# Kernel optimization log

Hardware: AMD Instinct MI355X
Metric: run time of the kernel (lower is better)

## Reference

```python
import jax, jax.numpy as jnp
import numpy as np

COUNT_CLIP_MAX = 1000.0

def _mlp2(x, w1, b1, w2, b2):
    # sg2im-style build_mlp with final_nonlinearity=True: relu after every linear
    h = jax.nn.relu(x @ w1 + b1)
    return jax.nn.relu(h @ w2 + b2)

def setup_inputs() -> dict:
    key = jax.random.key(0)
    ks = jax.random.split(key, 12)
    O, T, D, H = 100000, 400000, 128, 128
    D_out = D
    obj_vecs = jax.random.normal(ks[0], (O, D), dtype=jnp.float32)
    predi_vecs = jax.random.normal(ks[1], (T, D), dtype=jnp.float32)
    edges = jax.random.randint(ks[2], (T, 2), 0, O, dtype=jnp.int32)
    s = 0.02
    # net1: [3D, H, 2H + D_out]
    w1a = jax.random.normal(ks[3], (3 * D, H), dtype=jnp.float32) * s
    b1a = jnp.zeros((H,), dtype=jnp.float32)
    w1b = jax.random.normal(ks[4], (H, 2 * H + D_out), dtype=jnp.float32) * s
    b1b = jnp.zeros((2 * H + D_out,), dtype=jnp.float32)
    # net2: [H, H, D_out]
    w2a = jax.random.normal(ks[5], (H, H), dtype=jnp.float32) * s
    b2a = jnp.zeros((H,), dtype=jnp.float32)
    w2b = jax.random.normal(ks[6], (H, D_out), dtype=jnp.float32) * s
    b2b = jnp.zeros((D_out,), dtype=jnp.float32)
    return dict(obj_vecs=obj_vecs, predi_vecs=predi_vecs, edges=edges,
                w1a=w1a, b1a=b1a, w1b=w1b, b1b=b1b,
                w2a=w2a, b2a=b2a, w2b=w2b, b2b=b2b)

def reference(obj_vecs, predi_vecs, edges, w1a, b1a, w1b, b1b, w2a, b2a, w2b, b2b):
    O = obj_vecs.shape[0]
    H = w1a.shape[1]
    D_out = w2b.shape[1]
    s_idx = edges[:, 0]
    o_idx = edges[:, 1]
    # gather subject/object vectors, concat with predicate vecs: (T, 3D)
    cur_t_vecs = jnp.concatenate([obj_vecs[s_idx], predi_vecs, obj_vecs[o_idx]], axis=1)
    new_t_vecs = _mlp2(cur_t_vecs, w1a, b1a, w1b, b1b)  # (T, 2H + D_out)
    new_s_vecs = new_t_vecs[:, :H]
    new_p_vecs = new_t_vecs[:, H:H + D_out]
    new_o_vecs = new_t_vecs[:, H + D_out:2 * H + D_out]
    # scatter-add back to objects
    pooled = jnp.zeros((O, H), dtype=obj_vecs.dtype)
    pooled = pooled.at[s_idx].add(new_s_vecs).at[o_idx].add(new_o_vecs)
    # avg pooling: divide by clipped incidence counts
    ones = jnp.ones(s_idx.shape[0], dtype=obj_vecs.dtype)
    counts = jnp.zeros((O,), dtype=obj_vecs.dtype).at[s_idx].add(ones).at[o_idx].add(ones)
    counts = jnp.clip(counts, 1.0, COUNT_CLIP_MAX)
    pooled = pooled / counts[:, None]
    new_obj_vecs = _mlp2(pooled, w2a, b2a, w2b, b2b)  # (O, D_out)
    return new_obj_vecs, new_p_vecs
```

## Files before the change

### kernel.cpp

```cpp
#include <hip/hip_runtime.h>

typedef __attribute__((ext_vector_type(8))) short bf16x8;
typedef __attribute__((ext_vector_type(4))) float f32x4;
typedef __attribute__((ext_vector_type(4))) unsigned short u16x4;

#define MFMA __builtin_amdgcn_mfma_f32_16x16x32_bf16

__device__ __forceinline__ unsigned short f2bf(float x) {
    union { float f; unsigned u; } v; v.f = x;
    unsigned r = v.u + 0x7FFFu + ((v.u >> 16) & 1u);
    return (unsigned short)(r >> 16);
}
__device__ __forceinline__ float bf2f(unsigned short h) {
    union { unsigned u; float f; } v; v.u = ((unsigned)h) << 16;
    return v.f;
}

__global__ void pack_weights(const float* __restrict__ w1a, const float* __restrict__ w1b,
                             const float* __restrict__ w2a, const float* __restrict__ w2b,
                             unsigned short* __restrict__ pk)
{
    const int b = blockIdx.x, l = threadIdx.x;
    const float* W; int N, tile; unsigned short *ph, *pl;
    if (b < 96)       { W = w1a; N = 128; tile = b;       ph = pk;                 pl = pk + 96*512; }
    else if (b < 192) { W = w1b; N = 384; tile = b - 96;  ph = pk + 2*96*512;      pl = pk + 3*96*512; }
    else if (b < 224) { W = w2a; N = 128; tile = b - 192; ph = pk + 4*96*512;      pl = pk + 4*96*512 + 32*512; }
    else              { W = w2b; N = 128; tile = b - 224; ph = pk + 4*96*512 + 2*32*512; pl = pk + 4*96*512 + 3*32*512; }
    const int tpr = N / 16;
    const int kc = tile / tpr, ct = tile % tpr;
    bf16x8 hv, lv;
#pragma unroll
    for (int j = 0; j < 8; ++j) {
        int k = kc * 32 + (l >> 4) * 8 + j;
        int n = ct * 16 + (l & 15);
        float v = W[(size_t)k * N + n];
        unsigned short h = f2bf(v);
        hv[j] = (short)h;
        lv[j] = (short)f2bf(v - bf2f(h));
    }
    *(bf16x8*)&ph[(size_t)(tile * 64 + l) * 8] = hv;
    *(bf16x8*)&pl[(size_t)(tile * 64 + l) * 8] = lv;
}

__global__ __launch_bounds__(512, 4) void triple_mlp_mfma(
    const float* __restrict__ obj, const float* __restrict__ predi,
    const int* __restrict__ edges,
    const float* __restrict__ b1a, const float* __restrict__ b1b,
    const unsigned short* __restrict__ pk1a_h, const unsigned short* __restrict__ pk1a_l,
    const unsigned short* __restrict__ pk1b_h, const unsigned short* __restrict__ pk1b_l,
    float* __restrict__ pooled, float* __restrict__ out_p,
    float* __restrict__ counts, int T)
{
    __shared__ __align__(16) unsigned short Xh[64 * 128];
    __shared__ __align__(16) unsigned short Xl[64 * 128];
    __shared__ int sIdx[64], oIdx[64];

    const int tid = threadIdx.x;
    const int w = tid >> 6, l = tid & 63;
    const int rh = w & 1, cg = w >> 1;
    const int t0 = blockIdx.x * 64;

    if (tid < 64) {
        int t = t0 + tid; int tc = (t < T) ? t : (T - 1);
        sIdx[tid] = edges[2 * tc];
        oIdx[tid] = edges[2 * tc + 1];
    }
    __syncthreads();

    if (tid < 64)        { if (t0 + tid      < T) atomicAdd(&counts[sIdx[tid]],      1.0f); }
    else if (tid < 128)  { if (t0 + tid - 64 < T) atomicAdd(&counts[oIdx[tid - 64]], 1.0f); }

    f32x4 acc1[2][2];
#pragma unroll
    for (int i = 0; i < 2; ++i) { acc1[i][0] = (f32x4)0.0f; acc1[i][1] = (f32x4)0.0f; }

#pragma unroll
    for (int s = 0; s < 3; ++s) {
#pragma unroll
        for (int it = 0; it < 4; ++it) {
            int q = it * 512 + tid;
            int row = q >> 5, c4 = (q & 31) * 4;
            int t = t0 + row; int tc = (t < T) ? t : (T - 1);
            const float* src = (s == 0) ? obj   + (size_t)sIdx[row] * 128 + c4
                             : (s == 1) ? predi + (size_t)tc        * 128 + c4
                                        : obj   + (size_t)oIdx[row] * 128 + c4;
            float4 v = *(const float4*)src;
            u16x4 hv, lv;
            unsigned short h;
            h = f2bf(v.x); hv[0] = h; lv[0] = f2bf(v.x - bf2f(h));
            h = f2bf(v.y); hv[1] = h; lv[1] = f2bf(v.y - bf2f(h));
            h = f2bf(v.z); hv[2] = h; lv[2] = f2bf(v.z - bf2f(h));
            h = f2bf(v.w); hv[3] = h; lv[3] = f2bf(v.w - bf2f(h));
            int pc = row * 128 + (c4 ^ ((row & 7) << 3));
            *(u16x4*)&Xh[pc] = hv;
            *(u16x4*)&Xl[pc] = lv;
        }
        __syncthreads();

#pragma unroll
        for (int kc2 = 0; kc2 < 4; ++kc2) {
            const int kcg = s * 4 + kc2;
            bf16x8 ah[2], al[2];
#pragma unroll
            for (int rt = 0; rt < 2; ++rt) {
                int row = (rh * 2 + rt) * 16 + (l & 15);
                int col0 = kc2 * 32 + (l >> 4) * 8;
                int pc = row * 128 + (col0 ^ ((row & 7) << 3));
                ah[rt] = *(const bf16x8*)&Xh[pc];
                al[rt] = *(const bf16x8*)&Xl[pc];
            }
#pragma unroll
            for (int c2 = 0; c2 < 2; ++c2) {
                const int tile = kcg * 8 + cg * 2 + c2;
                bf16x8 bh = *(const bf16x8*)&pk1a_h[(size_t)(tile * 64 + l) * 8];
                bf16x8 bl = *(const bf16x8*)&pk1a_l[(size_t)(tile * 64 + l) * 8];
#pragma unroll
                for (int rt = 0; rt < 2; ++rt) {
                    acc1[rt][c2] = MFMA(ah[rt], bh, acc1[rt][c2], 0, 0, 0);
                    acc1[rt][c2] = MFMA(ah[rt], bl, acc1[rt][c2], 0, 0, 0);
                    acc1[rt][c2] = MFMA(al[rt], bh, acc1[rt][c2], 0, 0, 0);
                }
            }
        }
        __syncthreads();
    }

#pragma unroll
    for (int c2 = 0; c2 < 2; ++c2) {
        int col = cg * 32 + c2 * 16 + (l & 15);
        float bb = b1a[col];
#pragma unroll
        for (int rt = 0; rt < 2; ++rt) {
#pragma unroll
            for (int r = 0; r < 4; ++r) {
                int row = (rh * 2 + rt) * 16 + (l >> 4) * 4 + r;
                float h = fmaxf(acc1[rt][c2][r] + bb, 0.0f);
                unsigned short hh = f2bf(h);
                unsigned short hl = f2bf(h - bf2f(hh));
                int pc = row * 128 + (col ^ ((row & 7) << 3));
                Xh[pc] = hh; Xl[pc] = hl;
            }
        }
    }
    __syncthreads();

    f32x4 acc2[2][6];
#pragma unroll
    for (int i = 0; i < 2; ++i)
#pragma unroll
        for (int j = 0; j < 6; ++j) acc2[i][j] = (f32x4)0.0f;

#pragma unroll
    for (int kc = 0; kc < 4; ++kc) {
        bf16x8 ah[2], al[2];
#pragma unroll
        for (int rt = 0; rt < 2; ++rt) {
            int row = (rh * 2 + rt) * 16 + (l & 15);
            int col0 = kc * 32 + (l >> 4) * 8;
            int pc = row * 128 + (col0 ^ ((row & 7) << 3));
            ah[rt] = *(const bf16x8*)&Xh[pc];
            al[rt] = *(const bf16x8*)&Xl[pc];
        }
#pragma unroll
        for (int ct = 0; ct < 6; ++ct) {
            const int tile = kc * 24 + cg * 6 + ct;
            bf16x8 bh = *(const bf16x8*)&pk1b_h[(size_t)(tile * 64 + l) * 8];
            bf16x8 bl = *(const bf16x8*)&pk1b_l[(size_t)(tile * 64 + l) * 8];
#pragma unroll
            for (int rt = 0; rt < 2; ++rt) {
                acc2[rt][ct] = MFMA(ah[rt], bh, acc2[rt][ct], 0, 0, 0);
                acc2[rt][ct] = MFMA(ah[rt], bl, acc2[rt][ct], 0, 0, 0);
                acc2[rt][ct] = MFMA(al[rt], bh, acc2[rt][ct], 0, 0, 0);
            }
        }
    }

#pragma unroll
    for (int ct = 0; ct < 6; ++ct) {
        int col = cg * 96 + ct * 16 + (l & 15);
        float bb = b1b[col];
#pragma unroll
        for (int rt = 0; rt < 2; ++rt) {
#pragma unroll
            for (int r = 0; r < 4; ++r) {
                int row = (rh * 2 + rt) * 16 + (l >> 4) * 4 + r;
                if (t0 + row >= T) continue;
                float v = fmaxf(acc2[rt][ct][r] + bb, 0.0f);
                if (col < 128)
                    atomicAdd(&pooled[(size_t)sIdx[row] * 128 + col], v);
                else if (col < 256)
                    out_p[(size_t)(t0 + row) * 128 + (col - 128)] = v;
                else
                    atomicAdd(&pooled[(size_t)oIdx[row] * 128 + (col - 256)], v);
            }
        }
    }
}

__global__ __launch_bounds__(512, 4) void obj_mlp_mfma(
    const float* __restrict__ b2a, const float* __restrict__ b2b,
    const unsigned short* __restrict__ pk2a_h, const unsigned short* __restrict__ pk2a_l,
    const unsigned short* __restrict__ pk2b_h, const unsigned short* __restrict__ pk2b_l,
    float* __restrict__ io, const float* __restrict__ counts, int O)
{
    __shared__ __align__(16) unsigned short Xh[64 * 128];
    __shared__ __align__(16) unsigned short Xl[64 * 128];

    const int tid = threadIdx.x;
    const int w = tid >> 6, l = tid & 63;
    const int rh = w & 1, cg = w >> 1;
    const int r0 = blockIdx.x * 64;

#pragma unroll
    for (int it = 0; it < 4; ++it) {
        int q = it * 512 + tid;
        int row = q >> 5, c4 = (q & 31) * 4;
        int rg = r0 + row; if (rg > O - 1) rg = O - 1;
        float c = counts[rg];
        c = fminf(fmaxf(c, 1.0f), 1000.0f);
        float inv = 1.0f / c;
        float4 v = *(const float4*)&io[(size_t)rg * 128 + c4];
        v.x *= inv; v.y *= inv; v.z *= inv; v.w *= inv;
        u16x4 hv, lv;
        unsigned short h;
        h = f2bf(v.x); hv[0] = h; lv[0] = f2bf(v.x - bf2f(h));
        h = f2bf(v.y); hv[1] = h; lv[1] = f2bf(v.y - bf2f(h));
        h = f2bf(v.z); hv[2] = h; lv[2] = f2bf(v.z - bf2f(h));
        h = f2bf(v.w); hv[3] = h; lv[3] = f2bf(v.w - bf2f(h));
        int pc = row * 128 + (c4 ^ ((row & 7) << 3));
        *(u16x4*)&Xh[pc] = hv;
        *(u16x4*)&Xl[pc] = lv;
    }
    __syncthreads();

    f32x4 acc[2][2];
#pragma unroll
    for (int i = 0; i < 2; ++i) { acc[i][0] = (f32x4)0.0f; acc[i][1] = (f32x4)0.0f; }

#pragma unroll
    for (int kc = 0; kc < 4; ++kc) {
        bf16x8 ah[2], al[2];
#pragma unroll
        for (int rt = 0; rt < 2; ++rt) {
            int row = (rh * 2 + rt) * 16 + (l & 15);
            int col0 = kc * 32 + (l >> 4) * 8;
            int pc = row * 128 + (col0 ^ ((row & 7) << 3));
            ah[rt] = *(const bf16x8*)&Xh[pc];
            al[rt] = *(const bf16x8*)&Xl[pc];
        }
#pragma unroll
        for (int c2 = 0; c2 < 2; ++c2) {
            const int tile = kc * 8 + cg * 2 + c2;
            bf16x8 bh = *(const bf16x8*)&pk2a_h[(size_t)(tile * 64 + l) * 8];
            bf16x8 bl = *(const bf16x8*)&pk2a_l[(size_t)(tile * 64 + l) * 8];
#pragma unroll
            for (int rt = 0; rt < 2; ++rt) {
                acc[rt][c2] = MFMA(ah[rt], bh, acc[rt][c2], 0, 0, 0);
                acc[rt][c2] = MFMA(ah[rt], bl, acc[rt][c2], 0, 0, 0);
                acc[rt][c2] = MFMA(al[rt], bh, acc[rt][c2], 0, 0, 0);
            }
        }
    }
    __syncthreads();

#pragma unroll
    for (int c2 = 0; c2 < 2; ++c2) {
        int col = cg * 32 + c2 * 16 + (l & 15);
        float bb = b2a[col];
#pragma unroll
        for (int rt = 0; rt < 2; ++rt) {
#pragma unroll
            for (int r = 0; r < 4; ++r) {
                int row = (rh * 2 + rt) * 16 + (l >> 4) * 4 + r;
                float h = fmaxf(acc[rt][c2][r] + bb, 0.0f);
                unsigned short hh = f2bf(h);
                unsigned short hl = f2bf(h - bf2f(hh));
                int pc = row * 128 + (col ^ ((row & 7) << 3));
                Xh[pc] = hh; Xl[pc] = hl;
            }
        }
    }
    __syncthreads();

    f32x4 acc2[2][2];
#pragma unroll
    for (int i = 0; i < 2; ++i) { acc2[i][0] = (f32x4)0.0f; acc2[i][1] = (f32x4)0.0f; }

#pragma unroll
    for (int kc = 0; kc < 4; ++kc) {
        bf16x8 ah[2], al[2];
#pragma unroll
        for (int rt = 0; rt < 2; ++rt) {
            int row = (rh * 2 + rt) * 16 + (l & 15);
            int col0 = kc * 32 + (l >> 4) * 8;
            int pc = row * 128 + (col0 ^ ((row & 7) << 3));
            ah[rt] = *(const bf16x8*)&Xh[pc];
            al[rt] = *(const bf16x8*)&Xl[pc];
        }
#pragma unroll
        for (int c2 = 0; c2 < 2; ++c2) {
            const int tile = kc * 8 + cg * 2 + c2;
            bf16x8 bh = *(const bf16x8*)&pk2b_h[(size_t)(tile * 64 + l) * 8];
            bf16x8 bl = *(const bf16x8*)&pk2b_l[(size_t)(tile * 64 + l) * 8];
#pragma unroll
            for (int rt = 0; rt < 2; ++rt) {
                acc2[rt][c2] = MFMA(ah[rt], bh, acc2[rt][c2], 0, 0, 0);
                acc2[rt][c2] = MFMA(ah[rt], bl, acc2[rt][c2], 0, 0, 0);
                acc2[rt][c2] = MFMA(al[rt], bh, acc2[rt][c2], 0, 0, 0);
            }
        }
    }

#pragma unroll
    for (int c2 = 0; c2 < 2; ++c2) {
        int col = cg * 32 + c2 * 16 + (l & 15);
        float bb = b2b[col];
#pragma unroll
        for (int rt = 0; rt < 2; ++rt) {
#pragma unroll
            for (int r = 0; r < 4; ++r) {
                int row = (rh * 2 + rt) * 16 + (l >> 4) * 4 + r;
                if (r0 + row >= O) continue;
                float v = fmaxf(acc2[rt][c2][r] + bb, 0.0f);
                io[(size_t)(r0 + row) * 128 + col] = v;
            }
        }
    }
}

extern "C" void kernel_launch(void* const* d_in, const int* in_sizes, int n_in,
                              void* d_out, int out_size, void* d_ws, size_t ws_size,
                              hipStream_t stream) {
    const float* obj   = (const float*)d_in[0];
    const float* predi = (const float*)d_in[1];
    const int*   edges = (const int*)d_in[2];
    const float* w1a   = (const float*)d_in[3];
    const float* b1a   = (const float*)d_in[4];
    const float* w1b   = (const float*)d_in[5];
    const float* b1b   = (const float*)d_in[6];
    const float* w2a   = (const float*)d_in[7];
    const float* b2a   = (const float*)d_in[8];
    const float* w2b   = (const float*)d_in[9];
    const float* b2b   = (const float*)d_in[10];
    (void)n_in; (void)ws_size; (void)out_size;

    const int O = in_sizes[0] / 128;
    const int T = in_sizes[1] / 128;

    float* out    = (float*)d_out;
    float* pooled = out;
    float* out_p  = out + (size_t)O * 128;
    float* counts = (float*)d_ws;

    unsigned short* pk = (unsigned short*)(counts + O);
    unsigned short* pk1a_h = pk;
    unsigned short* pk1a_l = pk1a_h + 96 * 512;
    unsigned short* pk1b_h = pk1a_l + 96 * 512;
    unsigned short* pk1b_l = pk1b_h + 96 * 512;
    unsigned short* pk2a_h = pk1b_l + 96 * 512;
    unsigned short* pk2a_l = pk2a_h + 32 * 512;
    unsigned short* pk2b_h = pk2a_l + 32 * 512;
    unsigned short* pk2b_l = pk2b_h + 32 * 512;

    hipMemsetAsync(pooled, 0, (size_t)O * 128 * sizeof(float), stream);
    hipMemsetAsync(counts, 0, (size_t)O * sizeof(float), stream);

    pack_weights<<<256, 64, 0, stream>>>(w1a, w1b, w2a, w2b, pk);

    triple_mlp_mfma<<<(T + 63) / 64, 512, 0, stream>>>(
        obj, predi, edges, b1a, b1b,
        pk1a_h, pk1a_l, pk1b_h, pk1b_l,
        pooled, out_p, counts, T);

    obj_mlp_mfma<<<(O + 63) / 64, 512, 0, stream>>>(
        b2a, b2b, pk2a_h, pk2a_l, pk2b_h, pk2b_l,
        pooled, counts, O);
}
```

Measured before the change: 984.0 us.

## Precompute per-object first-layer projections and gather them per edge

Splits the first linear layer by input block: the subject and object parts of W1a are applied once per object in a new kernel, writing a per-object table. The edge kernel then gathers and sums these projections, adding only the predicate GEMM. This cuts the per-edge first-layer matmul work to a third. In exchange it adds a large workspace table write and read, and requires enough workspace, with a fallback to the old path otherwise.

```diff
diff --git a/kernel.cpp b/kernel.cpp
--- a/kernel.cpp
+++ b/kernel.cpp
@@ -14,6 +14,460 @@
 __device__ __forceinline__ float bf2f(unsigned short h) {
     union { unsigned u; float f; } v; v.u = ((unsigned)h) << 16;
     return v.f;
+}
+
+__global__ void pack_new(const float* __restrict__ w1a, const float* __restrict__ w1b,
+                         const float* __restrict__ w2a, const float* __restrict__ w2b,
+                         unsigned short* __restrict__ pk)
+{
+    const int b = blockIdx.x, l = threadIdx.x;
+    unsigned short* ph;
+    unsigned short* pl;
+    int tile;
+    bf16x8 hv, lv;
+
+    if (b < 64) {
+        tile = b;
+        ph = pk; pl = pk + 64 * 512;
+        int kc = tile >> 4, ct = tile & 15;
+#pragma unroll
+        for (int j = 0; j < 8; ++j) {
+            int k = kc * 32 + (l >> 4) * 8 + j;
+            int n = ct * 16 + (l & 15);
+            float v = (n < 128) ? w1a[(size_t)k * 128 + n]
+                                : w1a[(size_t)(256 + k) * 128 + (n - 128)];
+            unsigned short h = f2bf(v);
+            hv[j] = (short)h; lv[j] = (short)f2bf(v - bf2f(h));
+        }
+    } else if (b < 96) {
+        tile = b - 64;
+        ph = pk + 2 * 64 * 512; pl = ph + 32 * 512;
+        int kc = tile >> 3, ct = tile & 7;
+#pragma unroll
+        for (int j = 0; j < 8; ++j) {
+            int k = kc * 32 + (l >> 4) * 8 + j;
+            int n = ct * 16 + (l & 15);
+            float v = w1a[(size_t)(128 + k) * 128 + n];
+            unsigned short h = f2bf(v);
+            hv[j] = (short)h; lv[j] = (short)f2bf(v - bf2f(h));
+        }
+    } else if (b < 192) {
+        tile = b - 96;
+        ph = pk + 2 * 64 * 512 + 2 * 32 * 512; pl = ph + 96 * 512;
+        int kc = tile / 24, ct = tile % 24;
+#pragma unroll
+        for (int j = 0; j < 8; ++j) {
+            int k = kc * 32 + (l >> 4) * 8 + j;
+            int n = ct * 16 + (l & 15);
+            float v = w1b[(size_t)k * 384 + n];
+            unsigned short h = f2bf(v);
+            hv[j] = (short)h; lv[j] = (short)f2bf(v - bf2f(h));
+        }
+    } else if (b < 224) {
+        tile = b - 192;
+        ph = pk + 2 * 64 * 512 + 2 * 32 * 512 + 2 * 96 * 512; pl = ph + 32 * 512;
+        int kc = tile >> 3, ct = tile & 7;
+#pragma unroll
+        for (int j = 0; j < 8; ++j) {
+            int k = kc * 32 + (l >> 4) * 8 + j;
+            int n = ct * 16 + (l & 15);
+            float v = w2a[(size_t)k * 128 + n];
+            unsigned short h = f2bf(v);
+            hv[j] = (short)h; lv[j] = (short)f2bf(v - bf2f(h));
+        }
+    } else {
+        tile = b - 224;
+        ph = pk + 2 * 64 * 512 + 2 * 32 * 512 + 2 * 96 * 512 + 2 * 32 * 512; pl = ph + 32 * 512;
+        int kc = tile >> 3, ct = tile & 7;
+#pragma unroll
+        for (int j = 0; j < 8; ++j) {
+            int k = kc * 32 + (l >> 4) * 8 + j;
+            int n = ct * 16 + (l & 15);
+            float v = w2b[(size_t)k * 128 + n];
+            unsigned short h = f2bf(v);
+            hv[j] = (short)h; lv[j] = (short)f2bf(v - bf2f(h));
+        }
+    }
+    *(bf16x8*)&ph[(size_t)(tile * 64 + l) * 8] = hv;
+    *(bf16x8*)&pl[(size_t)(tile * 64 + l) * 8] = lv;
+}
+
+__global__ __launch_bounds__(512, 4) void obj_pre_kernel(
+    const float* __restrict__ obj,
+    const unsigned short* __restrict__ pkc_h, const unsigned short* __restrict__ pkc_l,
+    float* __restrict__ A_tb, int O)
+{
+    __shared__ __align__(16) unsigned short Xh[64 * 128];
+    __shared__ __align__(16) unsigned short Xl[64 * 128];
+
+    const int tid = threadIdx.x;
+    const int w = tid >> 6, l = tid & 63;
+    const int rh = w & 1, cg = w >> 1;
+    const int r0 = blockIdx.x * 64;
+
+#pragma unroll
+    for (int it = 0; it < 4; ++it) {
+        int q = it * 512 + tid;
+        int row = q >> 5, c4 = (q & 31) * 4;
+        int rg = r0 + row; if (rg > O - 1) rg = O - 1;
+        float4 v = *(const float4*)&obj[(size_t)rg * 128 + c4];
+        u16x4 hv, lv; unsigned short h;
+        h = f2bf(v.x); hv[0] = h; lv[0] = f2bf(v.x - bf2f(h));
+        h = f2bf(v.y); hv[1] = h; lv[1] = f2bf(v.y - bf2f(h));
+        h = f2bf(v.z); hv[2] = h; lv[2] = f2bf(v.z - bf2f(h));
+        h = f2bf(v.w); hv[3] = h; lv[3] = f2bf(v.w - bf2f(h));
+        int pc = row * 128 + (c4 ^ ((row & 7) << 3));
+        *(u16x4*)&Xh[pc] = hv;
+        *(u16x4*)&Xl[pc] = lv;
+    }
+    __syncthreads();
+
+    f32x4 acc[2][4];
+#pragma unroll
+    for (int i = 0; i < 2; ++i)
+#pragma unroll
+        for (int j = 0; j < 4; ++j) acc[i][j] = (f32x4)0.0f;
+
+#pragma unroll
+    for (int kc = 0; kc < 4; ++kc) {
+        bf16x8 ah[2], al[2];
+#pragma unroll
+        for (int rt = 0; rt < 2; ++rt) {
+            int row = (rh * 2 + rt) * 16 + (l & 15);
+            int col0 = kc * 32 + (l >> 4) * 8;
+            int pc = row * 128 + (col0 ^ ((row & 7) << 3));
+            ah[rt] = *(const bf16x8*)&Xh[pc];
+            al[rt] = *(const bf16x8*)&Xl[pc];
+        }
+#pragma unroll
+        for (int ct = 0; ct < 4; ++ct) {
+            const int tile = kc * 16 + cg * 4 + ct;
+            bf16x8 bh = *(const bf16x8*)&pkc_h[(size_t)(tile * 64 + l) * 8];
+            bf16x8 bl = *(const bf16x8*)&pkc_l[(size_t)(tile * 64 + l) * 8];
+#pragma unroll
+            for (int rt = 0; rt < 2; ++rt) {
+                acc[rt][ct] = MFMA(ah[rt], bh, acc[rt][ct], 0, 0, 0);
+                acc[rt][ct] = MFMA(ah[rt], bl, acc[rt][ct], 0, 0, 0);
+                acc[rt][ct] = MFMA(al[rt], bh, acc[rt][ct], 0, 0, 0);
+            }
+        }
+    }
+
+#pragma unroll
+    for (int ct = 0; ct < 4; ++ct) {
+        int col = cg * 64 + ct * 16 + (l & 15);
+#pragma unroll
+        for (int rt = 0; rt < 2; ++rt) {
+#pragma unroll
+            for (int r = 0; r < 4; ++r) {
+                int row = (rh * 2 + rt) * 16 + (l >> 4) * 4 + r;
+                if (r0 + row < O)
+                    A_tb[(size_t)(r0 + row) * 256 + col] = acc[rt][ct][r];
+            }
+        }
+    }
+}
+
+__global__ __launch_bounds__(512, 4) void triple_mlp_mfma2(
+    const float* __restrict__ A_tb, const float* __restrict__ predi,
+    const int* __restrict__ edges,
+    const float* __restrict__ b1a, const float* __restrict__ b1b,
+    const unsigned short* __restrict__ pkm_h, const unsigned short* __restrict__ pkm_l,
+    const unsigned short* __restrict__ pk1b_h, const unsigned short* __restrict__ pk1b_l,
+    float* __restrict__ pooled, float* __restrict__ out_p,
+    float* __restrict__ counts, int T)
+{
+    __shared__ __align__(16) char SB[64 * 132 * 4];
+    float (*G)[132] = (float (*)[132])SB;
+    unsigned short* Xh = (unsigned short*)SB;
+    unsigned short* Xl = (unsigned short*)(SB + 64 * 128 * 2);
+    __shared__ int sIdx[64], oIdx[64];
+
+    const int tid = threadIdx.x;
+    const int w = tid >> 6, l = tid & 63;
+    const int rh = w & 1, cg = w >> 1;
+    const int t0 = blockIdx.x * 64;
+
+    if (tid < 64) {
+        int t = t0 + tid; int tc = (t < T) ? t : (T - 1);
+        sIdx[tid] = edges[2 * tc];
+        oIdx[tid] = edges[2 * tc + 1];
+    }
+    __syncthreads();
+
+    if (tid < 64)        { if (t0 + tid      < T) atomicAdd(&counts[sIdx[tid]],      1.0f); }
+    else if (tid < 128)  { if (t0 + tid - 64 < T) atomicAdd(&counts[oIdx[tid - 64]], 1.0f); }
+
+#pragma unroll
+    for (int it = 0; it < 4; ++it) {
+        int q = it * 512 + tid;
+        int row = q >> 5, c4 = (q & 31) * 4;
+        float4 a = *(const float4*)&A_tb[(size_t)sIdx[row] * 256 + c4];
+        float4 b = *(const float4*)&A_tb[(size_t)oIdx[row] * 256 + 128 + c4];
+        float4 bb = *(const float4*)&b1a[c4];
+        float4 g;
+        g.x = a.x + b.x + bb.x; g.y = a.y + b.y + bb.y;
+        g.z = a.z + b.z + bb.z; g.w = a.w + b.w + bb.w;
+        *(float4*)&G[row][c4] = g;
+    }
+    __syncthreads();
+
+    f32x4 acc1[2][2];
+#pragma unroll
+    for (int rt = 0; rt < 2; ++rt)
+#pragma unroll
+        for (int c2 = 0; c2 < 2; ++c2) {
+            int col = cg * 32 + c2 * 16 + (l & 15);
+#pragma unroll
+            for (int r = 0; r < 4; ++r) {
+                int row = (rh * 2 + rt) * 16 + (l >> 4) * 4 + r;
+                acc1[rt][c2][r] = G[row][col];
+            }
+        }
+    __syncthreads();
+
+#pragma unroll
+    for (int it = 0; it < 4; ++it) {
+        int q = it * 512 + tid;
+        int row = q >> 5, c4 = (q & 31) * 4;
+        int t = t0 + row; int tc = (t < T) ? t : (T - 1);
+        float4 v = *(const float4*)&predi[(size_t)tc * 128 + c4];
+        u16x4 hv, lv; unsigned short h;
+        h = f2bf(v.x); hv[0] = h; lv[0] = f2bf(v.x - bf2f(h));
+        h = f2bf(v.y); hv[1] = h; lv[1] = f2bf(v.y - bf2f(h));
+        h = f2bf(v.z); hv[2] = h; lv[2] = f2bf(v.z - bf2f(h));
+        h = f2bf(v.w); hv[3] = h; lv[3] = f2bf(v.w - bf2f(h));
+        int pc = row * 128 + (c4 ^ ((row & 7) << 3));
+        *(u16x4*)&Xh[pc] = hv;
+        *(u16x4*)&Xl[pc] = lv;
+    }
+    __syncthreads();
+
+#pragma unroll
+    for (int kc = 0; kc < 4; ++kc) {
+        bf16x8 ah[2], al[2];
+#pragma unroll
+        for (int rt = 0; rt < 2; ++rt) {
+            int row = (rh * 2 + rt) * 16 + (l & 15);
+            int col0 = kc * 32 + (l >> 4) * 8;
+            int pc = row * 128 + (col0 ^ ((row & 7) << 3));
+            ah[rt] = *(const bf16x8*)&Xh[pc];
+            al[rt] = *(const bf16x8*)&Xl[pc];
+        }
+#pragma unroll
+        for (int c2 = 0; c2 < 2; ++c2) {
+            const int tile = kc * 8 + cg * 2 + c2;
+            bf16x8 bh = *(const bf16x8*)&pkm_h[(size_t)(tile * 64 + l) * 8];
+            bf16x8 bl = *(const bf16x8*)&pkm_l[(size_t)(tile * 64 + l) * 8];
+#pragma unroll
+            for (int rt = 0; rt < 2; ++rt) {
+                acc1[rt][c2] = MFMA(ah[rt], bh, acc1[rt][c2], 0, 0, 0);
+                acc1[rt][c2] = MFMA(ah[rt], bl, acc1[rt][c2], 0, 0, 0);
+                acc1[rt][c2] = MFMA(al[rt], bh, acc1[rt][c2], 0, 0, 0);
+            }
+        }
+    }
+    __syncthreads();
+
+#pragma unroll
+    for (int c2 = 0; c2 < 2; ++c2) {
+        int col = cg * 32 + c2 * 16 + (l & 15);
+#pragma unroll
+        for (int rt = 0; rt < 2; ++rt) {
+#pragma unroll
+            for (int r = 0; r < 4; ++r) {
+                int row = (rh * 2 + rt) * 16 + (l >> 4) * 4 + r;
+                float h = fmaxf(acc1[rt][c2][r], 0.0f);
+                unsigned short hh = f2bf(h);
+                unsigned short hl = f2bf(h - bf2f(hh));
+                int pc = row * 128 + (col ^ ((row & 7) << 3));
+                Xh[pc] = hh; Xl[pc] = hl;
+            }
+        }
+    }
+    __syncthreads();
+
+    f32x4 acc2[2][6];
+#pragma unroll
+    for (int i = 0; i < 2; ++i)
+#pragma unroll
+        for (int j = 0; j < 6; ++j) acc2[i][j] = (f32x4)0.0f;
+
+#pragma unroll
+    for (int kc = 0; kc < 4; ++kc) {
+        bf16x8 ah[2], al[2];
+#pragma unroll
+        for (int rt = 0; rt < 2; ++rt) {
+            int row = (rh * 2 + rt) * 16 + (l & 15);
+            int col0 = kc * 32 + (l >> 4) * 8;
+            int pc = row * 128 + (col0 ^ ((row & 7) << 3));
+            ah[rt] = *(const bf16x8*)&Xh[pc];
+            al[rt] = *(const bf16x8*)&Xl[pc];
+        }
+#pragma unroll
+        for (int ct = 0; ct < 6; ++ct) {
+            const int tile = kc * 24 + cg * 6 + ct;
+            bf16x8 bh = *(const bf16x8*)&pk1b_h[(size_t)(tile * 64 + l) * 8];
+            bf16x8 bl = *(const bf16x8*)&pk1b_l[(size_t)(tile * 64 + l) * 8];
+#pragma unroll
+            for (int rt = 0; rt < 2; ++rt) {
+                acc2[rt][ct] = MFMA(ah[rt], bh, acc2[rt][ct], 0, 0, 0);
+                acc2[rt][ct] = MFMA(ah[rt], bl, acc2[rt][ct], 0, 0, 0);
+                acc2[rt][ct] = MFMA(al[rt], bh, acc2[rt][ct], 0, 0, 0);
+            }
+        }
+    }
+
+#pragma unroll
+    for (int ct = 0; ct < 6; ++ct) {
+        int col = cg * 96 + ct * 16 + (l & 15);
+        float bb = b1b[col];
+#pragma unroll
+        for (int rt = 0; rt < 2; ++rt) {
+#pragma unroll
+            for (int r = 0; r < 4; ++r) {
+                int row = (rh * 2 + rt) * 16 + (l >> 4) * 4 + r;
+                if (t0 + row >= T) continue;
+                float v = fmaxf(acc2[rt][ct][r] + bb, 0.0f);
+                if (col < 128)
+                    atomicAdd(&pooled[(size_t)sIdx[row] * 128 + col], v);
+                else if (col < 256)
+                    out_p[(size_t)(t0 + row) * 128 + (col - 128)] = v;
+                else
+                    atomicAdd(&pooled[(size_t)oIdx[row] * 128 + (col - 256)], v);
+            }
+        }
+    }
+}
+
+__global__ __launch_bounds__(512, 4) void obj_mlp_mfma(
+    const float* __restrict__ b2a, const float* __restrict__ b2b,
+    const unsigned short* __restrict__ pk2a_h, const unsigned short* __restrict__ pk2a_l,
+    const unsigned short* __restrict__ pk2b_h, const unsigned short* __restrict__ pk2b_l,
+    float* __restrict__ io, const float* __restrict__ counts, int O)
+{
+    __shared__ __align__(16) unsigned short Xh[64 * 128];
+    __shared__ __align__(16) unsigned short Xl[64 * 128];
+
+    const int tid = threadIdx.x;
+    const int w = tid >> 6, l = tid & 63;
+    const int rh = w & 1, cg = w >> 1;
+    const int r0 = blockIdx.x * 64;
+
+#pragma unroll
+    for (int it = 0; it < 4; ++it) {
+        int q = it * 512 + tid;
+        int row = q >> 5, c4 = (q & 31) * 4;
+        int rg = r0 + row; if (rg > O - 1) rg = O - 1;
+        float c = counts[rg];
+        c = fminf(fmaxf(c, 1.0f), 1000.0f);
+        float inv = 1.0f / c;
+        float4 v = *(const float4*)&io[(size_t)rg * 128 + c4];
+        v.x *= inv; v.y *= inv; v.z *= inv; v.w *= inv;
+        u16x4 hv, lv; unsigned short h;
+        h = f2bf(v.x); hv[0] = h; lv[0] = f2bf(v.x - bf2f(h));
+        h = f2bf(v.y); hv[1] = h; lv[1] = f2bf(v.y - bf2f(h));
+        h = f2bf(v.z); hv[2] = h; lv[2] = f2bf(v.z - bf2f(h));
+        h = f2bf(v.w); hv[3] = h; lv[3] = f2bf(v.w - bf2f(h));
+        int pc = row * 128 + (c4 ^ ((row & 7) << 3));
+        *(u16x4*)&Xh[pc] = hv;
+        *(u16x4*)&Xl[pc] = lv;
+    }
+    __syncthreads();
+
+    f32x4 acc[2][2];
+#pragma unroll
+    for (int i = 0; i < 2; ++i) { acc[i][0] = (f32x4)0.0f; acc[i][1] = (f32x4)0.0f; }
+
+#pragma unroll
+    for (int kc = 0; kc < 4; ++kc) {
+        bf16x8 ah[2], al[2];
+#pragma unroll
+        for (int rt = 0; rt < 2; ++rt) {
+            int row = (rh * 2 + rt) * 16 + (l & 15);
+            int col0 = kc * 32 + (l >> 4) * 8;
+            int pc = row * 128 + (col0 ^ ((row & 7) << 3));
+            ah[rt] = *(const bf16x8*)&Xh[pc];
+            al[rt] = *(const bf16x8*)&Xl[pc];
+        }
+#pragma unroll
+        for (int c2 = 0; c2 < 2; ++c2) {
+            const int tile = kc * 8 + cg * 2 + c2;
+            bf16x8 bh = *(const bf16x8*)&pk2a_h[(size_t)(tile * 64 + l) * 8];
+            bf16x8 bl = *(const bf16x8*)&pk2a_l[(size_t)(tile * 64 + l) * 8];
+#pragma unroll
+            for (int rt = 0; rt < 2; ++rt) {
+                acc[rt][c2] = MFMA(ah[rt], bh, acc[rt][c2], 0, 0, 0);
+                acc[rt][c2] = MFMA(ah[rt], bl, acc[rt][c2], 0, 0, 0);
+                acc[rt][c2] = MFMA(al[rt], bh, acc[rt][c2], 0, 0, 0);
+            }
+        }
+    }
+    __syncthreads();
+
+#pragma unroll
+    for (int c2 = 0; c2 < 2; ++c2) {
+        int col = cg * 32 + c2 * 16 + (l & 15);
+        float bb = b2a[col];
+#pragma unroll
+        for (int rt = 0; rt < 2; ++rt) {
+#pragma unroll
+            for (int r = 0; r < 4; ++r) {
+                int row = (rh * 2 + rt) * 16 + (l >> 4) * 4 + r;
+                float h = fmaxf(acc[rt][c2][r] + bb, 0.0f);
+                unsigned short hh = f2bf(h);
+                unsigned short hl = f2bf(h - bf2f(hh));
+                int pc = row * 128 + (col ^ ((row & 7) << 3));
+                Xh[pc] = hh; Xl[pc] = hl;
+            }
+        }
+    }
+    __syncthreads();
+
+    f32x4 acc2[2][2];
+#pragma unroll
+    for (int i = 0; i < 2; ++i) { acc2[i][0] = (f32x4)0.0f; acc2[i][1] = (f32x4)0.0f; }
+
+#pragma unroll
+    for (int kc = 0; kc < 4; ++kc) {
+        bf16x8 ah[2], al[2];
+#pragma unroll
+        for (int rt = 0; rt < 2; ++rt) {
+            int row = (rh * 2 + rt) * 16 + (l & 15);
+            int col0 = kc * 32 + (l >> 4) * 8;
+            int pc = row * 128 + (col0 ^ ((row & 7) << 3));
+            ah[rt] = *(const bf16x8*)&Xh[pc];
+            al[rt] = *(const bf16x8*)&Xl[pc];
+        }
+#pragma unroll
+        for (int c2 = 0; c2 < 2; ++c2) {
+            const int tile = kc * 8 + cg * 2 + c2;
+            bf16x8 bh = *(const bf16x8*)&pk2b_h[(size_t)(tile * 64 + l) * 8];
+            bf16x8 bl = *(const bf16x8*)&pk2b_l[(size_t)(tile * 64 + l) * 8];
+#pragma unroll
+            for (int rt = 0; rt < 2; ++rt) {
+                acc2[rt][c2] = MFMA(ah[rt], bh, acc2[rt][c2], 0, 0, 0);
+                acc2[rt][c2] = MFMA(ah[rt], bl, acc2[rt][c2], 0, 0, 0);
+                acc2[rt][c2] = MFMA(al[rt], bh, acc2[rt][c2], 0, 0, 0);
+            }
+        }
+    }
+
+#pragma unroll
+    for (int c2 = 0; c2 < 2; ++c2) {
+        int col = cg * 32 + c2 * 16 + (l & 15);
+        float bb = b2b[col];
+#pragma unroll
+        for (int rt = 0; rt < 2; ++rt) {
+#pragma unroll
+            for (int r = 0; r < 4; ++r) {
+                int row = (rh * 2 + rt) * 16 + (l >> 4) * 4 + r;
+                if (r0 + row >= O) continue;
+                float v = fmaxf(acc2[rt][c2][r] + bb, 0.0f);
+                io[(size_t)(r0 + row) * 128 + col] = v;
+            }
+        }
+    }
 }
 
 __global__ void pack_weights(const float* __restrict__ w1a, const float* __restrict__ w1b,
@@ -85,8 +539,7 @@
                              : (s == 1) ? predi + (size_t)tc        * 128 + c4
                                         : obj   + (size_t)oIdx[row] * 128 + c4;
             float4 v = *(const float4*)src;
-            u16x4 hv, lv;
-            unsigned short h;
+            u16x4 hv, lv; unsigned short h;
             h = f2bf(v.x); hv[0] = h; lv[0] = f2bf(v.x - bf2f(h));
             h = f2bf(v.y); hv[1] = h; lv[1] = f2bf(v.y - bf2f(h));
             h = f2bf(v.z); hv[2] = h; lv[2] = f2bf(v.z - bf2f(h));
@@ -192,137 +645,6 @@
                     out_p[(size_t)(t0 + row) * 128 + (col - 128)] = v;
                 else
                     atomicAdd(&pooled[(size_t)oIdx[row] * 128 + (col - 256)], v);
-            }
-        }
-    }
-}
-
-__global__ __launch_bounds__(512, 4) void obj_mlp_mfma(
-    const float* __restrict__ b2a, const float* __restrict__ b2b,
-    const unsigned short* __restrict__ pk2a_h, const unsigned short* __restrict__ pk2a_l,
-    const unsigned short* __restrict__ pk2b_h, const unsigned short* __restrict__ pk2b_l,
-    float* __restrict__ io, const float* __restrict__ counts, int O)
-{
-    __shared__ __align__(16) unsigned short Xh[64 * 128];
-    __shared__ __align__(16) unsigned short Xl[64 * 128];
-
-    const int tid = threadIdx.x;
-    const int w = tid >> 6, l = tid & 63;
-    const int rh = w & 1, cg = w >> 1;
-    const int r0 = blockIdx.x * 64;
-
-#pragma unroll
-    for (int it = 0; it < 4; ++it) {
-        int q = it * 512 + tid;
-        int row = q >> 5, c4 = (q & 31) * 4;
-        int rg = r0 + row; if (rg > O - 1) rg = O - 1;
-        float c = counts[rg];
-        c = fminf(fmaxf(c, 1.0f), 1000.0f);
-        float inv = 1.0f / c;
-        float4 v = *(const float4*)&io[(size_t)rg * 128 + c4];
-        v.x *= inv; v.y *= inv; v.z *= inv; v.w *= inv;
-        u16x4 hv, lv;
-        unsigned short h;
-        h = f2bf(v.x); hv[0] = h; lv[0] = f2bf(v.x - bf2f(h));
-        h = f2bf(v.y); hv[1] = h; lv[1] = f2bf(v.y - bf2f(h));
-        h = f2bf(v.z); hv[2] = h; lv[2] = f2bf(v.z - bf2f(h));
-        h = f2bf(v.w); hv[3] = h; lv[3] = f2bf(v.w - bf2f(h));
-        int pc = row * 128 + (c4 ^ ((row & 7) << 3));
-        *(u16x4*)&Xh[pc] = hv;
-        *(u16x4*)&Xl[pc] = lv;
-    }
-    __syncthreads();
-
-    f32x4 acc[2][2];
-#pragma unroll
-    for (int i = 0; i < 2; ++i) { acc[i][0] = (f32x4)0.0f; acc[i][1] = (f32x4)0.0f; }
-
-#pragma unroll
-    for (int kc = 0; kc < 4; ++kc) {
-        bf16x8 ah[2], al[2];
-#pragma unroll
-        for (int rt = 0; rt < 2; ++rt) {
-            int row = (rh * 2 + rt) * 16 + (l & 15);
-            int col0 = kc * 32 + (l >> 4) * 8;
-            int pc = row * 128 + (col0 ^ ((row & 7) << 3));
-            ah[rt] = *(const bf16x8*)&Xh[pc];
-            al[rt] = *(const bf16x8*)&Xl[pc];
-        }
-#pragma unroll
-        for (int c2 = 0; c2 < 2; ++c2) {
-            const int tile = kc * 8 + cg * 2 + c2;
-            bf16x8 bh = *(const bf16x8*)&pk2a_h[(size_t)(tile * 64 + l) * 8];
-            bf16x8 bl = *(const bf16x8*)&pk2a_l[(size_t)(tile * 64 + l) * 8];
-#pragma unroll
-            for (int rt = 0; rt < 2; ++rt) {
-                acc[rt][c2] = MFMA(ah[rt], bh, acc[rt][c2], 0, 0, 0);
-                acc[rt][c2] = MFMA(ah[rt], bl, acc[rt][c2], 0, 0, 0);
-                acc[rt][c2] = MFMA(al[rt], bh, acc[rt][c2], 0, 0, 0);
-            }
-        }
-    }
-    __syncthreads();
-
-#pragma unroll
-    for (int c2 = 0; c2 < 2; ++c2) {
-        int col = cg * 32 + c2 * 16 + (l & 15);
-        float bb = b2a[col];
-#pragma unroll
-        for (int rt = 0; rt < 2; ++rt) {
-#pragma unroll
-            for (int r = 0; r < 4; ++r) {
-                int row = (rh * 2 + rt) * 16 + (l >> 4) * 4 + r;
-                float h = fmaxf(acc[rt][c2][r] + bb, 0.0f);
-                unsigned short hh = f2bf(h);
-                unsigned short hl = f2bf(h - bf2f(hh));
-                int pc = row * 128 + (col ^ ((row & 7) << 3));
-                Xh[pc] = hh; Xl[pc] = hl;
-            }
-        }
-    }
-    __syncthreads();
-
-    f32x4 acc2[2][2];
-#pragma unroll
-    for (int i = 0; i < 2; ++i) { acc2[i][0] = (f32x4)0.0f; acc2[i][1] = (f32x4)0.0f; }
-
-#pragma unroll
-    for (int kc = 0; kc < 4; ++kc) {
-        bf16x8 ah[2], al[2];
-#pragma unroll
-        for (int rt = 0; rt < 2; ++rt) {
-            int row = (rh * 2 + rt) * 16 + (l & 15);
-            int col0 = kc * 32 + (l >> 4) * 8;
-            int pc = row * 128 + (col0 ^ ((row & 7) << 3));
-            ah[rt] = *(const bf16x8*)&Xh[pc];
-            al[rt] = *(const bf16x8*)&Xl[pc];
-        }
-#pragma unroll
-        for (int c2 = 0; c2 < 2; ++c2) {
-            const int tile = kc * 8 + cg * 2 + c2;
-            bf16x8 bh = *(const bf16x8*)&pk2b_h[(size_t)(tile * 64 + l) * 8];
-            bf16x8 bl = *(const bf16x8*)&pk2b_l[(size_t)(tile * 64 + l) * 8];
-#pragma unroll
-            for (int rt = 0; rt < 2; ++rt) {
-                acc2[rt][c2] = MFMA(ah[rt], bh, acc2[rt][c2], 0, 0, 0);
-                acc2[rt][c2] = MFMA(ah[rt], bl, acc2[rt][c2], 0, 0, 0);
-                acc2[rt][c2] = MFMA(al[rt], bh, acc2[rt][c2], 0, 0, 0);
-            }
-        }
-    }
-
-#pragma unroll
-    for (int c2 = 0; c2 < 2; ++c2) {
-        int col = cg * 32 + c2 * 16 + (l & 15);
-        float bb = b2b[col];
-#pragma unroll
-        for (int rt = 0; rt < 2; ++rt) {
-#pragma unroll
-            for (int r = 0; r < 4; ++r) {
-                int row = (rh * 2 + rt) * 16 + (l >> 4) * 4 + r;
-                if (r0 + row >= O) continue;
-                float v = fmaxf(acc2[rt][c2][r] + bb, 0.0f);
-                io[(size_t)(r0 + row) * 128 + col] = v;
             }
         }
     }
@@ -342,7 +664,7 @@
     const float* b2a   = (const float*)d_in[8];
     const float* w2b   = (const float*)d_in[9];
     const float* b2b   = (const float*)d_in[10];
-    (void)n_in; (void)ws_size; (void)out_size;
+    (void)n_in; (void)out_size;
 
     const int O = in_sizes[0] / 128;
     const int T = in_sizes[1] / 128;
@@ -351,28 +673,50 @@
     float* pooled = out;
     float* out_p  = out + (size_t)O * 128;
     float* counts = (float*)d_ws;
-
     unsigned short* pk = (unsigned short*)(counts + O);
-    unsigned short* pk1a_h = pk;
-    unsigned short* pk1a_l = pk1a_h + 96 * 512;
-    unsigned short* pk1b_h = pk1a_l + 96 * 512;
-    unsigned short* pk1b_l = pk1b_h + 96 * 512;
-    unsigned short* pk2a_h = pk1b_l + 96 * 512;
-    unsigned short* pk2a_l = pk2a_h + 32 * 512;
-    unsigned short* pk2b_h = pk2a_l + 32 * 512;
-    unsigned short* pk2b_l = pk2b_h + 32 * 512;
 
     hipMemsetAsync(pooled, 0, (size_t)O * 128 * sizeof(float), stream);
     hipMemsetAsync(counts, 0, (size_t)O * sizeof(float), stream);
 
-    pack_weights<<<256, 64, 0, stream>>>(w1a, w1b, w2a, w2b, pk);
-
-    triple_mlp_mfma<<<(T + 63) / 64, 512, 0, stream>>>(
-        obj, predi, edges, b1a, b1b,
-        pk1a_h, pk1a_l, pk1b_h, pk1b_l,
-        pooled, out_p, counts, T);
-
-    obj_mlp_mfma<<<(O + 63) / 64, 512, 0, stream>>>(
-        b2a, b2b, pk2a_h, pk2a_l, pk2b_h, pk2b_l,
-        pooled, counts, O);
-}
+    const size_t need = (size_t)O * 4 + (size_t)512 * 512 * 2 + (size_t)O * 256 * 4;
+
+    if (ws_size >= need) {
+        unsigned short* pkc_h  = pk;
+        unsigned short* pkc_l  = pkc_h  + 64 * 512;
+        unsigned short* pkm_h  = pkc_l  + 64 * 512;
+        unsigned short* pkm_l  = pkm_h  + 32 * 512;
+        unsigned short* pk1b_h = pkm_l  + 32 * 512;
+        unsigned short* pk1b_l = pk1b_h + 96 * 512;
+        unsigned short* pk2a_h = pk1b_l + 96 * 512;
+        unsigned short* pk2a_l = pk2a_h + 32 * 512;
+        unsigned short* pk2b_h = pk2a_l + 32 * 512;
+        unsigned short* pk2b_l = pk2b_h + 32 * 512;
+        float* A_tb = (float*)(pk + (size_t)512 * 512);
+
+        pack_new<<<256, 64, 0, stream>>>(w1a, w1b, w2a, w2b, pk);
+        obj_pre_kernel<<<(O + 63) / 64, 512, 0, stream>>>(obj, pkc_h, pkc_l, A_tb, O);
+        triple_mlp_mfma2<<<(T + 63) / 64, 512, 0, stream>>>(
+            A_tb, predi, edges, b1a, b1b,
+            pkm_h, pkm_l, pk1b_h, pk1b_l,
+            pooled, out_p, counts, T);
+        obj_mlp_mfma<<<(O + 63) / 64, 512, 0, stream>>>(
+            b2a, b2b, pk2a_h, pk2a_l, pk2b_h, pk2b_l, pooled, counts, O);
+    } else {
+        unsigned short* pk1a_h = pk;
+        unsigned short* pk1a_l = pk1a_h + 96 * 512;
+        unsigned short* pk1b_h = pk1a_l + 96 * 512;
+        unsigned short* pk1b_l = pk1b_h + 96 * 512;
+        unsigned short* pk2a_h = pk1b_l + 96 * 512;
+        unsigned short* pk2a_l = pk2a_h + 32 * 512;
+        unsigned short* pk2b_h = pk2a_l + 32 * 512;
+        unsigned short* pk2b_l = pk2b_h + 32 * 512;
+
+        pack_weights<<<256, 64, 0, stream>>>(w1a, w1b, w2a, w2b, pk);
+        triple_mlp_mfma<<<(T + 63) / 64, 512, 0, stream>>>(
+            obj, predi, edges, b1a, b1b,
+            pk1a_h, pk1a_l, pk1b_h, pk1b_l,
+            pooled, out_p, counts, T);
+        obj_mlp_mfma<<<(O + 63) / 64, 512, 0, stream>>>(
+            b2a, b2b, pk2a_h, pk2a_l, pk2b_h, pk2b_l, pooled, counts, O);
+    }
+}
```

New measurement: 1.028 ms. 1.05x slower.
